# Performance work log

Measured on AMD Instinct MI355X. Metric: run time of the kernel, lower is better.

Reference implementation:

```python
import jax, jax.numpy as jnp
import numpy as np
from jax import lax

UNIT = 0.11  # pairing threshold from sort_w(weight, 0.11)


def _greedy_pairs(wflat, unit=UNIT):
    """Faithful greedy pairing from sort_w: for each out-channel dd, scan flat
    indices a ascending; pair a with the first unoccupied b>a with
    |w[a]+w[b]|<=unit. Returns gather indices src and signs such that
    Weff[dd,i] = sign[dd,i] * Wflat[dd, src[dd,i]] reproduces vicsum_v2."""
    d, m = wflat.shape
    src = np.tile(np.arange(m, dtype=np.int32), (d, 1))
    sign = np.ones((d, m), dtype=np.float32)
    for dd in range(d):
        occ = np.zeros(m, dtype=bool)
        row = wflat[dd]
        for a in range(m - 1):
            if occ[a]:
                continue
            cand = np.nonzero((~occ[a + 1:]) & (np.abs(row[a] + row[a + 1:]) <= unit))[0]
            if cand.size:
                b = a + 1 + int(cand[0])
                occ[a] = occ[b] = True
                src[dd, b] = a     # out += (x[a]-x[b])*w[a]  =>  coeff at b is -w[a]
                sign[dd, b] = -1.0
    return src, sign


def _make_conv(rng, d, c, k):
    bound = 1.0 / np.sqrt(c * k * k)  # torch default uniform init scale
    w = rng.uniform(-bound, bound, size=(d, c, k, k)).astype(np.float32)
    b = rng.uniform(-bound, bound, size=(d,)).astype(np.float32)
    src, sign = _greedy_pairs(w.reshape(d, -1))
    return w, b, src, sign


def setup_inputs() -> dict:
    rng = np.random.default_rng(0)
    x = rng.standard_normal((16384, 1, 32, 32)).astype(np.float32)
    w1, b1, src1, sign1 = _make_conv(rng, 6, 1, 5)
    w2, b2, src2, sign2 = _make_conv(rng, 16, 6, 5)
    w3, b3, src3, sign3 = _make_conv(rng, 120, 16, 5)
    bf1 = 1.0 / np.sqrt(120.0)
    fc1_w = rng.uniform(-bf1, bf1, size=(84, 120)).astype(np.float32)
    fc1_b = rng.uniform(-bf1, bf1, size=(84,)).astype(np.float32)
    bf2 = 1.0 / np.sqrt(84.0)
    fc2_w = rng.uniform(-bf2, bf2, size=(10, 84)).astype(np.float32)
    fc2_b = rng.uniform(-bf2, bf2, size=(10,)).astype(np.float32)
    return {
        'x': jnp.asarray(x),
        'w1': jnp.asarray(w1), 'b1': jnp.asarray(b1), 'sign1': jnp.asarray(sign1),
        'w2': jnp.asarray(w2), 'b2': jnp.asarray(b2), 'sign2': jnp.asarray(sign2),
        'w3': jnp.asarray(w3), 'b3': jnp.asarray(b3), 'sign3': jnp.asarray(sign3),
        'fc1_w': jnp.asarray(fc1_w), 'fc1_b': jnp.asarray(fc1_b),
        'fc2_w': jnp.asarray(fc2_w), 'fc2_b': jnp.asarray(fc2_b),
        'src1': jnp.asarray(src1), 'src2': jnp.asarray(src2), 'src3': jnp.asarray(src3),
        'TRIGGERed': 1, 'count': 0,
    }


def _eff_weight(w, src, sign):
    d = w.shape[0]
    wflat = w.reshape(d, -1)
    weff = jnp.take_along_axis(wflat, src, axis=1) * sign
    return weff.reshape(w.shape)


def _conv(x, w, b):
    y = lax.conv_general_dilated(x, w, window_strides=(1, 1), padding='VALID',
                                 dimension_numbers=('NCHW', 'OIHW', 'NCHW'))
    return y + b[None, :, None, None]


def _avgpool2(x):
    n, c, h, w = x.shape
    return x.reshape(n, c, h // 2, 2, w // 2, 2).mean(axis=(3, 5))


def reference(x, w1, b1, sign1, w2, b2, sign2, w3, b3, sign3,
              fc1_w, fc1_b, fc2_w, fc2_b, src1, src2, src3, TRIGGERed, count):
    if TRIGGERed:
        h = _avgpool2(jax.nn.sigmoid(_conv(x, _eff_weight(w1, src1, sign1), b1)))
        h = _avgpool2(jax.nn.sigmoid(_conv(h, _eff_weight(w2, src2, sign2), b2)))
        h = jax.nn.sigmoid(_conv(h, _eff_weight(w3, src3, sign3), b3))
    else:
        h = _avgpool2(jax.nn.sigmoid(_conv(x, w1, b1)))
        h = _avgpool2(jax.nn.sigmoid(_conv(h, w2, b2)))
        h = jax.nn.sigmoid(_conv(h, w3, b3))
    h = h.reshape(h.shape[0], -1)                     # [N, 120]
    h = jax.nn.sigmoid(h @ fc1_w.T + fc1_b)           # [N, 84]
    return h @ fc2_w.T + fc2_b                        # [N, 10]
```

## Files before the change

kernel.cpp:

```cpp
#include <hip/hip_runtime.h>

#define THREADS 256

__device__ __forceinline__ float sigmoidf(float x) {
    return __builtin_amdgcn_rcpf(1.0f + __expf(-x));
}

#define E2OFF 168
#define E3OFF 2856
#define P1OFF 54056

__global__ void weff_prep(const float* __restrict__ w1, const float* __restrict__ sg1, const int* __restrict__ sr1,
                          const float* __restrict__ w2, const float* __restrict__ sg2, const int* __restrict__ sr2,
                          const float* __restrict__ w3, const float* __restrict__ sg3, const int* __restrict__ sr3,
                          const int* __restrict__ trig, float* __restrict__ ws) {
    int i = blockIdx.x * blockDim.x + threadIdx.x;
    const int t = trig[0];
    if (i < 168) {
        int c = i / 28, k = i % 28;
        float v = 0.f;
        if (k < 25) { int f = c * 25 + k; v = t ? sg1[f] * w1[c * 25 + sr1[f]] : w1[f]; }
        ws[i] = v;
    } else if (i < E3OFF) {
        int j = i - E2OFF;
        int oc = j / 168, r = j % 168, ic = r / 28, k = r % 28;
        float v = 0.f;
        if (k < 25) { int f = oc * 150 + ic * 25 + k; v = t ? sg2[f] * w2[oc * 150 + sr2[f]] : w2[f]; }
        ws[i] = v;
    } else if (i < P1OFF) {
        int idx = i - E3OFF;
        int j  = idx & 3;
        int l  = (idx >> 2) & 63;
        int kw = idx >> 8;
        int k  = kw % 50, wt = kw / 50;
        int c  = (wt << 5) | (l >> 1);
        int h  = l & 1;
        float v = 0.f;
        if (c < 120) {
            int e = c * 400 + h * 200 + k * 4 + j;
            v = t ? sg3[e] * w3[c * 400 + sr3[e]] : w3[e];
        }
        ws[i] = v;
    }
}

__global__ __launch_bounds__(THREADS, 4)
void k_conv1(const float* __restrict__ x, const float* __restrict__ ws,
             const float* __restrict__ b1, float* __restrict__ p1, int nimg) {
    __shared__ __align__(16) float lw[176];
    const int tid = threadIdx.x;
    if (tid < 168) lw[tid] = ws[tid];
    if (tid >= 168 && tid < 174) lw[tid] = b1[tid - 168];
    __syncthreads();

    int g = blockIdx.x * THREADS + tid;
    if (g >= nimg * 98) return;
    const int img = g / 98, rem = g % 98;
    const int r = rem / 7, t = rem % 7;

    const float* xb = x + (size_t)img * 1024 + (2 * r) * 32 + 4 * t;
    float pt[6][8];
    #pragma unroll
    for (int rr = 0; rr < 6; ++rr) {
        const float4 v0 = *reinterpret_cast<const float4*>(xb + rr * 32);
        const float4 v1 = *reinterpret_cast<const float4*>(xb + rr * 32 + 4);
        pt[rr][0] = v0.x; pt[rr][1] = v0.y; pt[rr][2] = v0.z; pt[rr][3] = v0.w;
        pt[rr][4] = v1.x; pt[rr][5] = v1.y; pt[rr][6] = v1.z; pt[rr][7] = v1.w;
    }

    #pragma unroll
    for (int c = 0; c < 6; ++c) {
        float z[2][4];
        #pragma unroll
        for (int p = 0; p < 2; ++p)
            #pragma unroll
            for (int w = 0; w < 4; ++w) z[p][w] = 0.f;

        #pragma unroll
        for (int k4 = 0; k4 < 6; ++k4) {
            const float4 w4 = *reinterpret_cast<const float4*>(&lw[c * 28 + 4 * k4]);
            #pragma unroll
            for (int j = 0; j < 4; ++j) {
                const int k = 4 * k4 + j;
                const int ky = k / 5, kx = k % 5;
                const float wv = (j == 0) ? w4.x : (j == 1) ? w4.y : (j == 2) ? w4.z : w4.w;
                #pragma unroll
                for (int p = 0; p < 2; ++p)
                    #pragma unroll
                    for (int dy = 0; dy < 2; ++dy)
                        #pragma unroll
                        for (int dx = 0; dx < 2; ++dx)
                            z[p][2 * dy + dx] += pt[dy + ky][2 * p + dx + kx] * wv;
            }
        }
        {
            const float wv = lw[c * 28 + 24];
            #pragma unroll
            for (int p = 0; p < 2; ++p)
                #pragma unroll
                for (int dy = 0; dy < 2; ++dy)
                    #pragma unroll
                    for (int dx = 0; dx < 2; ++dx)
                        z[p][2 * dy + dx] += pt[dy + 4][2 * p + dx + 4] * wv;
        }

        const float bb = lw[168 + c];
        const float s0 = sigmoidf(z[0][0] + bb) + sigmoidf(z[0][1] + bb) +
                         sigmoidf(z[0][2] + bb) + sigmoidf(z[0][3] + bb);
        const float s1 = sigmoidf(z[1][0] + bb) + sigmoidf(z[1][1] + bb) +
                         sigmoidf(z[1][2] + bb) + sigmoidf(z[1][3] + bb);
        *reinterpret_cast<float2*>(&p1[((size_t)img * 6 + c) * 196 + r * 14 + 2 * t]) =
            make_float2(0.25f * s0, 0.25f * s1);
    }
}

__global__ __launch_bounds__(THREADS, 3)
void k_conv2(const float* __restrict__ p1, const float* __restrict__ ws,
             const float* __restrict__ b2, float* __restrict__ p2, int nimg) {
    int g = blockIdx.x * THREADS + threadIdx.x;
    if (g >= nimg * 50) return;
    const int img = g / 50, rem = g % 50;
    const int pix = rem >> 1, di = rem & 1;
    const int pi = pix / 5, pj = pix % 5;
    const float* pimg = p1 + (size_t)img * 1176 + (2 * pi + di) * 14 + 2 * pj;
    const float* wq = ws + E2OFF;

    float acc[16][2];
    #pragma unroll
    for (int oc = 0; oc < 16; ++oc) { acc[oc][0] = 0.f; acc[oc][1] = 0.f; }

    for (int ic = 0; ic < 6; ++ic) {
        float pt[5][6];
        const float* pb = pimg + ic * 196;
        #pragma unroll
        for (int r = 0; r < 5; ++r) {
            #pragma unroll
            for (int cc = 0; cc < 3; ++cc) {
                float2 v = *reinterpret_cast<const float2*>(pb + r * 14 + 2 * cc);
                pt[r][2 * cc] = v.x; pt[r][2 * cc + 1] = v.y;
            }
        }
        #pragma unroll
        for (int oc = 0; oc < 16; ++oc) {
            const float* wr = wq + oc * 168 + ic * 28;
            #pragma unroll
            for (int k4 = 0; k4 < 6; ++k4) {
                const float4 w4 = *reinterpret_cast<const float4*>(wr + 4 * k4);
                #pragma unroll
                for (int j = 0; j < 4; ++j) {
                    const int k = 4 * k4 + j;
                    const int ky = k / 5, kx = k % 5;
                    const float wv = (j == 0) ? w4.x : (j == 1) ? w4.y : (j == 2) ? w4.z : w4.w;
                    acc[oc][0] += pt[ky][kx] * wv;
                    acc[oc][1] += pt[ky][kx + 1] * wv;
                }
            }
            const float wv = wr[24];
            acc[oc][0] += pt[4][4] * wv;
            acc[oc][1] += pt[4][5] * wv;
        }
    }

    #pragma unroll
    for (int oc = 0; oc < 16; ++oc) {
        const float bb = b2[oc];
        float s = sigmoidf(acc[oc][0] + bb) + sigmoidf(acc[oc][1] + bb);
        s += __shfl_xor(s, 1, 64);
        if (di == 0)
            p2[(size_t)img * 400 + oc * 25 + pix] = 0.25f * s;
    }
}

#define K3_IMG 8
__global__ __launch_bounds__(THREADS, 4)
void k_tail(const float* __restrict__ p2, const float* __restrict__ ws,
            const float* __restrict__ b3,
            const float* __restrict__ fc1w, const float* __restrict__ fc1b,
            const float* __restrict__ fc2w, const float* __restrict__ fc2b,
            float* __restrict__ out, int nimg) {
    __shared__ __align__(16) float sp2[K3_IMG][400];
    __shared__ __align__(16) float v3[K3_IMG][120];
    __shared__ __align__(16) float v4[K3_IMG][84];
    const int tid = threadIdx.x;
    const int img0 = blockIdx.x * K3_IMG;

    for (int i = tid; i < K3_IMG * 100; i += THREADS) {
        const int im = i / 100, off = i % 100;
        const int gi = min(img0 + im, nimg - 1);
        reinterpret_cast<float4*>(&sp2[im][0])[off] =
            reinterpret_cast<const float4*>(p2 + (size_t)gi * 400)[off];
    }
    __syncthreads();

    if (tid < 240) {
        const int h = tid & 1;
        const int wt = tid >> 6, l = tid & 63;
        const float4* wp = reinterpret_cast<const float4*>(ws + E3OFF);
        float4 a[K3_IMG];
        #pragma unroll
        for (int im = 0; im < K3_IMG; ++im) a[im] = make_float4(0.f, 0.f, 0.f, 0.f);
        #pragma unroll 5
        for (int k = 0; k < 50; ++k) {
            const float4 w4 = wp[(wt * 50 + k) * 64 + l];
            #pragma unroll
            for (int im = 0; im < K3_IMG; ++im) {
                const float4 u = *reinterpret_cast<const float4*>(&sp2[im][h * 200 + 4 * k]);
                a[im].x += u.x * w4.x; a[im].y += u.y * w4.y;
                a[im].z += u.z * w4.z; a[im].w += u.w * w4.w;
            }
        }
        const int c = tid >> 1;
        #pragma unroll
        for (int im = 0; im < K3_IMG; ++im) {
            float z = (a[im].x + a[im].y) + (a[im].z + a[im].w);
            z += __shfl_xor(z, 1, 64);
            if (h == 0) v3[im][c] = sigmoidf(z + b3[c]);
        }
    }
    __syncthreads();

    for (int it = tid; it < K3_IMG * 84; it += THREADS) {
        const int im = it / 84, j = it % 84;
        const float4* wp = reinterpret_cast<const float4*>(fc1w + j * 120);
        const float4* vp = reinterpret_cast<const float4*>(&v3[im][0]);
        float4 a = make_float4(0.f, 0.f, 0.f, 0.f);
        #pragma unroll 6
        for (int k = 0; k < 30; ++k) {
            const float4 w4 = wp[k];
            const float4 u = vp[k];
            a.x += u.x * w4.x; a.y += u.y * w4.y;
            a.z += u.z * w4.z; a.w += u.w * w4.w;
        }
        v4[im][j] = sigmoidf((a.x + a.y) + (a.z + a.w) + fc1b[j]);
    }
    __syncthreads();

    if (tid < K3_IMG * 10) {
        const int im = tid / 10, j = tid % 10;
        if (img0 + im < nimg) {
            const float4* wp = reinterpret_cast<const float4*>(fc2w + j * 84);
            const float4* vp = reinterpret_cast<const float4*>(&v4[im][0]);
            float4 a = make_float4(0.f, 0.f, 0.f, 0.f);
            #pragma unroll
            for (int k = 0; k < 21; ++k) {
                const float4 w4 = wp[k];
                const float4 u = vp[k];
                a.x += u.x * w4.x; a.y += u.y * w4.y;
                a.z += u.z * w4.z; a.w += u.w * w4.w;
            }
            out[(size_t)(img0 + im) * 10 + j] = (a.x + a.y) + (a.z + a.w) + fc2b[j];
        }
    }
}

__device__ __forceinline__ float wget_ig(const float* __restrict__ wp,
                                         const float* __restrict__ sg,
                                         const int* __restrict__ sr,
                                         int row, int m, int idx, bool tg) {
    int f = row * m + idx;
    return tg ? sg[f] * wp[row * m + sr[f]] : wp[f];
}

__global__ __launch_bounds__(THREADS, 4)
void lenet_fused(const float* __restrict__ x,
                 const float* __restrict__ w1e, const float* __restrict__ b1,
                 const float* __restrict__ w2e, const float* __restrict__ b2,
                 const float* __restrict__ w3e, const float* __restrict__ b3,
                 const float* __restrict__ fc1w, const float* __restrict__ fc1b,
                 const float* __restrict__ fc2w, const float* __restrict__ fc2b,
                 const float* __restrict__ sg1, const int* __restrict__ sr1,
                 const float* __restrict__ sg2, const int* __restrict__ sr2,
                 const float* __restrict__ sg3, const int* __restrict__ sr3,
                 const int* __restrict__ trig,
                 float* __restrict__ out, int nimg) {
    const int tid = threadIdx.x;
    const int img0 = blockIdx.x * 2;
    __shared__ __align__(16) float xs[2][1024];
    __shared__ __align__(16) float p1[2][6][196];
    __shared__ __align__(16) float p2[2][400];
    __shared__ __align__(16) float v3[2][120];
    __shared__ __align__(16) float v4[2][84];
    const bool tg = trig[0] != 0;

    #pragma unroll
    for (int im = 0; im < 2; ++im) {
        int gi = min(img0 + im, nimg - 1);
        reinterpret_cast<float4*>(&xs[im][0])[tid] =
            reinterpret_cast<const float4*>(x + (size_t)gi * 1024)[tid];
    }
    __syncthreads();

    for (int it = tid; it < 2 * 196; it += THREADS) {
        const int img = it / 196, pix = it % 196;
        const int pi = pix / 14, pj = pix % 14;
        const float* xb = &xs[img][(2 * pi) * 32 + 2 * pj];
        float pt[6][6];
        #pragma unroll
        for (int r = 0; r < 6; ++r)
            #pragma unroll
            for (int cc = 0; cc < 3; ++cc) {
                float2 v = *reinterpret_cast<const float2*>(&xb[r * 32 + cc * 2]);
                pt[r][cc * 2] = v.x; pt[r][cc * 2 + 1] = v.y;
            }
        #pragma unroll
        for (int c = 0; c < 6; ++c) {
            float z0 = 0.f, z1 = 0.f, z2 = 0.f, z3 = 0.f;
            #pragma unroll
            for (int ky = 0; ky < 5; ++ky)
                #pragma unroll
                for (int kx = 0; kx < 5; ++kx) {
                    const float wv = wget_ig(w1e, sg1, sr1, c, 25, ky * 5 + kx, tg);
                    z0 += pt[ky][kx] * wv;     z1 += pt[ky][kx + 1] * wv;
                    z2 += pt[ky + 1][kx] * wv; z3 += pt[ky + 1][kx + 1] * wv;
                }
            const float bb = b1[c];
            p1[img][c][pix] = 0.25f * (sigmoidf(z0 + bb) + sigmoidf(z1 + bb) +
                                       sigmoidf(z2 + bb) + sigmoidf(z3 + bb));
        }
    }
    __syncthreads();

    if (tid < 200) {
        const int img = tid / 100, rem = tid % 100;
        const int pix = rem >> 2, win = rem & 3;
        const int di = win >> 1, dj = win & 1;
        const int pi = pix / 5, pj = pix % 5;
        const int r0 = 2 * pi + di, c0 = 2 * pj + dj;
        float acc[16];
        #pragma unroll
        for (int c = 0; c < 16; ++c) acc[c] = 0.f;
        for (int ic = 0; ic < 6; ++ic) {
            float pt[5][5];
            #pragma unroll
            for (int ky = 0; ky < 5; ++ky)
                #pragma unroll
                for (int kx = 0; kx < 5; ++kx)
                    pt[ky][kx] = p1[img][ic][(r0 + ky) * 14 + (c0 + kx)];
            #pragma unroll
            for (int c = 0; c < 16; ++c) {
                float z = acc[c];
                #pragma unroll
                for (int ky = 0; ky < 5; ++ky)
                    #pragma unroll
                    for (int kx = 0; kx < 5; ++kx)
                        z += pt[ky][kx] * wget_ig(w2e, sg2, sr2, c, 150, ic * 25 + ky * 5 + kx, tg);
                acc[c] = z;
            }
        }
        #pragma unroll
        for (int c = 0; c < 16; ++c) {
            float z = sigmoidf(acc[c] + b2[c]);
            z += __shfl_xor(z, 1, 64);
            z += __shfl_xor(z, 2, 64);
            if (win == 0) p2[img][c * 25 + pix] = 0.25f * z;
        }
    }
    __syncthreads();

    if (tid < 240) {
        const int c = tid >> 1, h = tid & 1;
        float s0 = 0.f, s1 = 0.f;
        for (int k = 0; k < 200; ++k) {
            float wv = wget_ig(w3e, sg3, sr3, c, 400, h * 200 + k, tg);
            s0 += p2[0][h * 200 + k] * wv;
            s1 += p2[1][h * 200 + k] * wv;
        }
        s0 += __shfl_xor(s0, 1, 64);
        s1 += __shfl_xor(s1, 1, 64);
        if (h == 0) {
            const float bb = b3[c];
            v3[0][c] = sigmoidf(s0 + bb);
            v3[1][c] = sigmoidf(s1 + bb);
        }
    }
    __syncthreads();

    if (tid < 168) {
        const int img = tid / 84, j = tid % 84;
        float a = 0.f;
        for (int k = 0; k < 120; ++k) a += v3[img][k] * fc1w[j * 120 + k];
        v4[img][j] = sigmoidf(a + fc1b[j]);
    }
    __syncthreads();

    if (tid < 20) {
        const int img = tid / 10, j = tid % 10;
        if (img0 + img < nimg) {
            float a = 0.f;
            for (int k = 0; k < 84; ++k) a += v4[img][k] * fc2w[j * 84 + k];
            out[(size_t)(img0 + img) * 10 + j] = a + fc2b[j];
        }
    }
}

extern "C" void kernel_launch(void* const* d_in, const int* in_sizes, int n_in,
                              void* d_out, int out_size, void* d_ws, size_t ws_size,
                              hipStream_t stream) {
    const float* x    = (const float*)d_in[0];
    const float* w1   = (const float*)d_in[1];
    const float* b1   = (const float*)d_in[2];
    const float* sg1  = (const float*)d_in[3];
    const float* w2   = (const float*)d_in[4];
    const float* b2   = (const float*)d_in[5];
    const float* sg2  = (const float*)d_in[6];
    const float* w3   = (const float*)d_in[7];
    const float* b3   = (const float*)d_in[8];
    const float* sg3  = (const float*)d_in[9];
    const float* fc1w = (const float*)d_in[10];
    const float* fc1b = (const float*)d_in[11];
    const float* fc2w = (const float*)d_in[12];
    const float* fc2b = (const float*)d_in[13];
    const int*   sr1  = (const int*)d_in[14];
    const int*   sr2  = (const int*)d_in[15];
    const int*   sr3  = (const int*)d_in[16];
    const int*   trig = (const int*)d_in[17];

    const int nimg = in_sizes[0] / 1024;
    float* out = (float*)d_out;

    const size_t p1off = P1OFF;
    const size_t p2off = p1off + (size_t)nimg * 1176;
    const size_t need_bytes = (p2off + (size_t)nimg * 400) * sizeof(float);

    if (ws_size >= need_bytes) {
        float* ws = (float*)d_ws;
        weff_prep<<<(P1OFF + 255) / 256, 256, 0, stream>>>(
            w1, sg1, sr1, w2, sg2, sr2, w3, sg3, sr3, trig, ws);
        k_conv1<<<(nimg * 98 + THREADS - 1) / THREADS, THREADS, 0, stream>>>(
            x, ws, b1, ws + p1off, nimg);
        k_conv2<<<(nimg * 50 + THREADS - 1) / THREADS, THREADS, 0, stream>>>(
            ws + p1off, ws, b2, ws + p2off, nimg);
        k_tail<<<(nimg + K3_IMG - 1) / K3_IMG, THREADS, 0, stream>>>(
            ws + p2off, ws, b3, fc1w, fc1b, fc2w, fc2b, out, nimg);
    } else {
        lenet_fused<<<(nimg + 1) / 2, THREADS, 0, stream>>>(
            x, w1, b1, w2, b2, w3, b3,
            fc1w, fc1b, fc2w, fc2b, sg1, sr1, sg2, sr2, sg3, sr3, trig, out, nimg);
    }
}
```

Baseline: 230.6 us.

## Give each conv3 thread two output channels and halve tail block size

The conv3 weight layout in the workspace is reshuffled so each thread reads two channels' float4 weights per k step. The tail kernel now runs with 128 threads, and 120 of them each compute two channels for 8 images, so every shared-memory activation load feeds twice as many FMAs. This is meant to cut LDS traffic per FMA and trim idle threads. In exchange each block has fewer threads doing the fc layers, and there is more register pressure. conv2's ic loop also gets an unroll-2 pragma.

```diff
diff --git a/kernel.cpp b/kernel.cpp
--- a/kernel.cpp
+++ b/kernel.cpp
@@ -29,18 +29,18 @@
         ws[i] = v;
     } else if (i < P1OFF) {
         int idx = i - E3OFF;
-        int j  = idx & 3;
-        int l  = (idx >> 2) & 63;
-        int kw = idx >> 8;
-        int k  = kw % 50, wt = kw / 50;
-        int c  = (wt << 5) | (l >> 1);
-        int h  = l & 1;
-        float v = 0.f;
-        if (c < 120) {
-            int e = c * 400 + h * 200 + k * 4 + j;
-            v = t ? sg3[e] * w3[c * 400 + sr3[e]] : w3[e];
-        }
-        ws[i] = v;
+        if (idx < 48000) {
+            int q  = idx & 3;
+            int j  = (idx >> 2) & 1;
+            int tt = (idx >> 3) % 120;
+            int k  = idx / 960;
+            int c  = 2 * (tt >> 1) + j;
+            int h  = tt & 1;
+            int e  = c * 400 + h * 200 + 4 * k + q;
+            ws[i] = t ? sg3[e] * w3[c * 400 + sr3[e]] : w3[e];
+        } else {
+            ws[i] = 0.f;
+        }
     }
 }
 
@@ -129,6 +129,7 @@
     #pragma unroll
     for (int oc = 0; oc < 16; ++oc) { acc[oc][0] = 0.f; acc[oc][1] = 0.f; }
 
+    #pragma unroll 2
     for (int ic = 0; ic < 6; ++ic) {
         float pt[5][6];
         const float* pb = pimg + ic * 196;
@@ -171,20 +172,20 @@
     }
 }
 
-#define K3_IMG 8
-__global__ __launch_bounds__(THREADS, 4)
+#define T_IMG 8
+__global__ __launch_bounds__(128, 4)
 void k_tail(const float* __restrict__ p2, const float* __restrict__ ws,
             const float* __restrict__ b3,
             const float* __restrict__ fc1w, const float* __restrict__ fc1b,
             const float* __restrict__ fc2w, const float* __restrict__ fc2b,
             float* __restrict__ out, int nimg) {
-    __shared__ __align__(16) float sp2[K3_IMG][400];
-    __shared__ __align__(16) float v3[K3_IMG][120];
-    __shared__ __align__(16) float v4[K3_IMG][84];
+    __shared__ __align__(16) float sp2[T_IMG][400];
+    __shared__ __align__(16) float v3[T_IMG][120];
+    __shared__ __align__(16) float v4[T_IMG][84];
     const int tid = threadIdx.x;
-    const int img0 = blockIdx.x * K3_IMG;
-
-    for (int i = tid; i < K3_IMG * 100; i += THREADS) {
+    const int img0 = blockIdx.x * T_IMG;
+
+    for (int i = tid; i < T_IMG * 100; i += 128) {
         const int im = i / 100, off = i % 100;
         const int gi = min(img0 + im, nimg - 1);
         reinterpret_cast<float4*>(&sp2[im][0])[off] =
@@ -192,34 +193,42 @@
     }
     __syncthreads();
 
-    if (tid < 240) {
+    if (tid < 120) {
         const int h = tid & 1;
-        const int wt = tid >> 6, l = tid & 63;
+        const int cpair = tid >> 1;
+        float acc[2][T_IMG];
+        #pragma unroll
+        for (int j = 0; j < 2; ++j)
+            #pragma unroll
+            for (int im = 0; im < T_IMG; ++im) acc[j][im] = 0.f;
+
         const float4* wp = reinterpret_cast<const float4*>(ws + E3OFF);
-        float4 a[K3_IMG];
-        #pragma unroll
-        for (int im = 0; im < K3_IMG; ++im) a[im] = make_float4(0.f, 0.f, 0.f, 0.f);
-        #pragma unroll 5
+        #pragma unroll 2
         for (int k = 0; k < 50; ++k) {
-            const float4 w4 = wp[(wt * 50 + k) * 64 + l];
-            #pragma unroll
-            for (int im = 0; im < K3_IMG; ++im) {
+            const float4 w0 = wp[(k * 120 + tid) * 2];
+            const float4 w1 = wp[(k * 120 + tid) * 2 + 1];
+            #pragma unroll
+            for (int im = 0; im < T_IMG; ++im) {
                 const float4 u = *reinterpret_cast<const float4*>(&sp2[im][h * 200 + 4 * k]);
-                a[im].x += u.x * w4.x; a[im].y += u.y * w4.y;
-                a[im].z += u.z * w4.z; a[im].w += u.w * w4.w;
-            }
-        }
-        const int c = tid >> 1;
-        #pragma unroll
-        for (int im = 0; im < K3_IMG; ++im) {
-            float z = (a[im].x + a[im].y) + (a[im].z + a[im].w);
-            z += __shfl_xor(z, 1, 64);
-            if (h == 0) v3[im][c] = sigmoidf(z + b3[c]);
-        }
-    }
-    __syncthreads();
-
-    for (int it = tid; it < K3_IMG * 84; it += THREADS) {
+                acc[0][im] += w0.x * u.x + w0.y * u.y + w0.z * u.z + w0.w * u.w;
+                acc[1][im] += w1.x * u.x + w1.y * u.y + w1.z * u.z + w1.w * u.w;
+            }
+        }
+        #pragma unroll
+        for (int j = 0; j < 2; ++j) {
+            const int c = 2 * cpair + j;
+            const float bb = b3[c];
+            #pragma unroll
+            for (int im = 0; im < T_IMG; ++im) {
+                float s = acc[j][im];
+                s += __shfl_xor(s, 1, 64);
+                if (h == 0) v3[im][c] = sigmoidf(s + bb);
+            }
+        }
+    }
+    __syncthreads();
+
+    for (int it = tid; it < T_IMG * 84; it += 128) {
         const int im = it / 84, j = it % 84;
         const float4* wp = reinterpret_cast<const float4*>(fc1w + j * 120);
         const float4* vp = reinterpret_cast<const float4*>(&v3[im][0]);
@@ -235,7 +244,7 @@
     }
     __syncthreads();
 
-    if (tid < K3_IMG * 10) {
+    if (tid < T_IMG * 10) {
         const int im = tid / 10, j = tid % 10;
         if (img0 + im < nimg) {
             const float4* wp = reinterpret_cast<const float4*>(fc2w + j * 84);
@@ -430,7 +439,7 @@
             x, ws, b1, ws + p1off, nimg);
         k_conv2<<<(nimg * 50 + THREADS - 1) / THREADS, THREADS, 0, stream>>>(
             ws + p1off, ws, b2, ws + p2off, nimg);
-        k_tail<<<(nimg + K3_IMG - 1) / K3_IMG, THREADS, 0, stream>>>(
+        k_tail<<<(nimg + T_IMG - 1) / T_IMG, 128, 0, stream>>>(
             ws + p2off, ws, b3, fc1w, fc1b, fc2w, fc2b, out, nimg);
     } else {
         lenet_fused<<<(nimg + 1) / 2, THREADS, 0, stream>>>(
```

After: 228.8 us. No clear change (-0.8%).
